# Optimization experiments

Hardware: AMD Instinct MI355X
Metric: run time of the kernel (lower is better)

Reference implementation:

```python
import jax, jax.numpy as jnp
import numpy as np

N_NODES = 100000
N_EDGES = 800000
DIMS = [(768, 64), (64, 32), (32, 16), (16, 5)]


def setup_inputs() -> dict:
    key = jax.random.key(0)
    ks = jax.random.split(key, 3 + 3 * len(DIMS))
    inp = {
        "x": jax.random.normal(ks[0], (N_NODES, DIMS[0][0]), jnp.float32),
        "edge_index": jax.random.randint(ks[1], (2, N_EDGES), 0, N_NODES),
        "edge_weight": jax.random.uniform(ks[2], (N_EDGES,), jnp.float32),
    }
    for i, (di, do) in enumerate(DIMS, start=1):
        s = 1.0 / np.sqrt(di)
        k0, k1, k2 = ks[3 * i], ks[3 * i + 1], ks[3 * i + 2]
        inp[f"W{i}l"] = jax.random.uniform(k0, (di, do), jnp.float32, -s, s)
        inp[f"W{i}r"] = jax.random.uniform(k1, (di, do), jnp.float32, -s, s)
        inp[f"b{i}"] = jax.random.uniform(k2, (do,), jnp.float32, -s, s)
    return inp


def _sage_conv(h, src, dst, inv_deg, Wl, Wr, b):
    # SAGEConv (mean aggregation): lin_l(mean_{j->i} h_j) + lin_r(h_i)
    agg = jax.ops.segment_sum(h[src], dst, num_segments=h.shape[0]) * inv_deg[:, None]
    return agg @ Wl + h @ Wr + b


def reference(x, edge_index, edge_weight,
              W1l, W1r, b1, W2l, W2r, b2, W3l, W3r, b3, W4l, W4r, b4):
    # edge_weight is accepted (matches original forward) but PyG SAGEConv mean
    # aggregation ignores it. Dropout is identity (deterministic eval reference).
    src, dst = edge_index[0], edge_index[1]
    deg = jax.ops.segment_sum(jnp.ones((src.shape[0],), x.dtype), dst,
                              num_segments=x.shape[0])
    inv_deg = jnp.where(deg > 0, 1.0 / deg, 0.0)
    h = jax.nn.relu(_sage_conv(x, src, dst, inv_deg, W1l, W1r, b1))
    h = jax.nn.relu(_sage_conv(h, src, dst, inv_deg, W2l, W2r, b2))
    h = jax.nn.relu(_sage_conv(h, src, dst, inv_deg, W3l, W3r, b3))
    return _sage_conv(h, src, dst, inv_deg, W4l, W4r, b4)
```

## Files before the change

kernel.cpp:

```cpp
#include <hip/hip_runtime.h>

using half8 = __attribute__((ext_vector_type(8))) _Float16;
using f32x4 = __attribute__((ext_vector_type(4))) float;

typedef __attribute__((address_space(3))) unsigned int lds_uint;
typedef __attribute__((address_space(1))) const unsigned int glb_uint;
__device__ __forceinline__ void async_copy16(const void* g, void* l) {
  __builtin_amdgcn_global_load_lds((glb_uint*)g, (lds_uint*)l, 16, 0, 0);
}

__device__ __forceinline__ void raw_barrier() {
  asm volatile("" ::: "memory");
  __builtin_amdgcn_s_barrier();
  asm volatile("" ::: "memory");
}

__global__ void zero_kernel(int4* __restrict__ p, int n4) {
  int i = blockIdx.x * 256 + threadIdx.x;
  if (i < n4) p[i] = make_int4(0, 0, 0, 0);
}

__global__ void prep_all_kernel(const float* __restrict__ W1l, const float* __restrict__ W1r,
                                const float* __restrict__ W2l, const float* __restrict__ W2r,
                                const float* __restrict__ W3l, const float* __restrict__ W3r,
                                const float* __restrict__ W4l, const float* __restrict__ W4r,
                                _Float16* __restrict__ w1, _Float16* __restrict__ w2,
                                _Float16* __restrict__ w3, _Float16* __restrict__ w4) {
  int i = blockIdx.x * 256 + threadIdx.x;
  if (i < 98304) {
    int c = i / 768, k = i - c * 768;
    float v = (c < 64) ? W1l[k * 64 + c] : W1r[k * 64 + (c - 64)];
    w1[i] = (_Float16)v;
  } else if (i < 98304 + 4096) {
    int j = i - 98304;
    int c = j >> 6, k = j & 63;
    float v = (c < 32) ? W2l[k * 32 + c] : W2r[k * 32 + (c - 32)];
    w2[j] = (_Float16)v;
  } else if (i < 98304 + 4096 + 1024) {
    int j = i - (98304 + 4096);
    int c = j >> 5, k = j & 31;
    float v = (c < 16) ? W3l[k * 16 + c] : W3r[k * 16 + (c - 16)];
    w3[j] = (_Float16)v;
  } else if (i < 98304 + 4096 + 1024 + 512) {
    int j = i - (98304 + 4096 + 1024);
    int c = j >> 5, k = j & 31;
    float v = 0.f;
    if (k < 16) {
      if (c < 5) v = W4l[k * 5 + c];
      else if (c < 10) v = W4r[k * 5 + (c - 5)];
    }
    w4[j] = (_Float16)v;
  }
}

__global__ void deg_kernel(const int* __restrict__ dst, int* __restrict__ cnt, int e) {
  int i = blockIdx.x * 256 + threadIdx.x;
  if (i < e) atomicAdd(&cnt[dst[i]], 1);
}

__global__ void scan1_kernel(const int* __restrict__ cnt, int* __restrict__ off,
                             int* __restrict__ bsum, float* __restrict__ invd, int nodes) {
  __shared__ int sh[256];
  int tid = threadIdx.x;
  int base = blockIdx.x * 1024 + tid * 4;
  int a0 = (base + 0 < nodes) ? cnt[base + 0] : 0;
  int a1 = (base + 1 < nodes) ? cnt[base + 1] : 0;
  int a2 = (base + 2 < nodes) ? cnt[base + 2] : 0;
  int a3 = (base + 3 < nodes) ? cnt[base + 3] : 0;
  if (base + 0 < nodes) invd[base + 0] = a0 > 0 ? 1.0f / (float)a0 : 0.f;
  if (base + 1 < nodes) invd[base + 1] = a1 > 0 ? 1.0f / (float)a1 : 0.f;
  if (base + 2 < nodes) invd[base + 2] = a2 > 0 ? 1.0f / (float)a2 : 0.f;
  if (base + 3 < nodes) invd[base + 3] = a3 > 0 ? 1.0f / (float)a3 : 0.f;
  int s3 = a0 + a1 + a2 + a3;
  sh[tid] = s3;
  __syncthreads();
  for (int d = 1; d < 256; d <<= 1) {
    int v = (tid >= d) ? sh[tid - d] : 0;
    __syncthreads();
    sh[tid] += v;
    __syncthreads();
  }
  int excl = sh[tid] - s3;
  if (base + 0 <= nodes) off[base + 0] = excl;
  if (base + 1 <= nodes) off[base + 1] = excl + a0;
  if (base + 2 <= nodes) off[base + 2] = excl + a0 + a1;
  if (base + 3 <= nodes) off[base + 3] = excl + a0 + a1 + a2;
  if (tid == 255) bsum[blockIdx.x] = sh[255];
}

__global__ void scan2_kernel(int* __restrict__ bsum, int nb) {
  __shared__ int sh[128];
  int tid = threadIdx.x;
  int v = (tid < nb) ? bsum[tid] : 0;
  sh[tid] = v;
  __syncthreads();
  for (int d = 1; d < 128; d <<= 1) {
    int u = (tid >= d) ? sh[tid - d] : 0;
    __syncthreads();
    sh[tid] += u;
    __syncthreads();
  }
  if (tid < nb) bsum[tid] = sh[tid] - v;
}

__global__ void scan3_kernel(int* __restrict__ off, const int* __restrict__ bsum, int ntot) {
  int i = blockIdx.x * 256 + threadIdx.x;
  if (i < ntot) off[i] += bsum[i >> 10];
}

__global__ void sortfill_kernel(const int* __restrict__ src, const int* __restrict__ dst,
                                const int* __restrict__ off, int* __restrict__ cur,
                                int* __restrict__ csr, int e) {
  int i = blockIdx.x * 256 + threadIdx.x;
  if (i < e) {
    int d = dst[i];
    int pos = atomicAdd(&cur[d], 1);
    csr[off[d] + pos] = src[i];
  }
}

__global__ __launch_bounds__(256, 3) void gemm1_kernel(
    const float* __restrict__ x,
    const _Float16* __restrict__ w16,
    const float* __restrict__ bias,
    _Float16* __restrict__ p, _Float16* __restrict__ q, int n) {
  constexpr int DI = 768, BK = 32, NT = DI / BK;
  __shared__ float aS[2][128 * BK];
  __shared__ _Float16 bS[2][128 * BK];
  int t = threadIdx.x;
  int lane = t & 63, w = t >> 6;
  int lm = lane & 15, lk = lane >> 4;
  int m0 = blockIdx.x * 128;

  const float* agp[4];
  int abase[4];
#pragma unroll
  for (int j = 0; j < 4; ++j) {
    int g = (j * 4 + w) * 64 + lane;
    int row = g >> 3, gi = g & 7;
    int gj = gi ^ (row & 7);
    int grow = m0 + row;
    if (grow >= n) grow = n - 1;
    agp[j] = x + (size_t)grow * DI + gj * 4;
    abase[j] = (j * 4 + w) * 256;
  }
  const _Float16* bgp[2];
  int bbase[2];
#pragma unroll
  for (int j = 0; j < 2; ++j) {
    int g = (j * 4 + w) * 64 + lane;
    int c = g >> 2, gi = g & 3;
    int gj = gi ^ ((c >> 1) & 3);
    bgp[j] = w16 + (size_t)c * DI + gj * 8;
    bbase[j] = (j * 4 + w) * 512;
  }

  f32x4 acc[2][8];
#pragma unroll
  for (int mi = 0; mi < 2; ++mi)
#pragma unroll
    for (int ni = 0; ni < 8; ++ni) acc[mi][ni] = (f32x4){0.f, 0.f, 0.f, 0.f};

  int r0l = w * 32 + lm, r1l = r0l + 16;
  int sw = lm & 7;
  int bsw = (lk ^ ((lm >> 1) & 3)) << 3;

  auto compute_tile = [&](const float* ab, const _Float16* bb) {
    f32x4 v0a = *(const f32x4*)(ab + r0l * 32 + (((lk * 2 + 0) ^ sw) << 2));
    f32x4 v0b = *(const f32x4*)(ab + r0l * 32 + (((lk * 2 + 1) ^ sw) << 2));
    f32x4 v1a = *(const f32x4*)(ab + r1l * 32 + (((lk * 2 + 0) ^ sw) << 2));
    f32x4 v1b = *(const f32x4*)(ab + r1l * 32 + (((lk * 2 + 1) ^ sw) << 2));
    half8 a0, a1;
#pragma unroll
    for (int j = 0; j < 4; ++j) {
      a0[j] = (_Float16)v0a[j]; a0[4 + j] = (_Float16)v0b[j];
      a1[j] = (_Float16)v1a[j]; a1[4 + j] = (_Float16)v1b[j];
    }
#pragma unroll
    for (int ni = 0; ni < 8; ++ni) {
      half8 b = *(const half8*)(bb + ni * 512 + lm * 32 + bsw);
      acc[0][ni] = __builtin_amdgcn_mfma_f32_16x16x32_f16(a0, b, acc[0][ni], 0, 0, 0);
      acc[1][ni] = __builtin_amdgcn_mfma_f32_16x16x32_f16(a1, b, acc[1][ni], 0, 0, 0);
    }
  };

#pragma unroll
  for (int j = 0; j < 4; ++j) async_copy16(agp[j], &aS[0][abase[j]]);
#pragma unroll
  for (int j = 0; j < 2; ++j) async_copy16(bgp[j], &bS[0][bbase[j]]);

  for (int ts = 0; ts < NT - 1; ++ts) {
    int cur = ts & 1;
    int kc = (ts + 1) * BK;
#pragma unroll
    for (int j = 0; j < 4; ++j) async_copy16(agp[j] + kc, &aS[cur ^ 1][abase[j]]);
#pragma unroll
    for (int j = 0; j < 2; ++j) async_copy16(bgp[j] + kc, &bS[cur ^ 1][bbase[j]]);
    asm volatile("s_waitcnt vmcnt(6)" ::: "memory");
    raw_barrier();
    compute_tile(aS[cur], bS[cur]);
    raw_barrier();
  }
  asm volatile("s_waitcnt vmcnt(0)" ::: "memory");
  raw_barrier();
  compute_tile(aS[(NT - 1) & 1], bS[(NT - 1) & 1]);

#pragma unroll
  for (int mi = 0; mi < 2; ++mi)
#pragma unroll
    for (int ni = 0; ni < 8; ++ni) {
      int col = ni * 16 + lm;
#pragma unroll
      for (int j = 0; j < 4; ++j) {
        int row = m0 + w * 32 + mi * 16 + lk * 4 + j;
        if (row < n) {
          float v = acc[mi][ni][j];
          if (col < 64) p[(size_t)row * 64 + col] = (_Float16)v;
          else q[(size_t)row * 64 + (col - 64)] = (_Float16)(v + bias[col - 64]);
        }
      }
    }
}

template <int DIR, int DIP, int PSI, int NC, int NCR, int DO, int PSO>
__global__ __launch_bounds__(256) void fused_agg_gemm_kernel(
    const _Float16* __restrict__ pin, const _Float16* __restrict__ qin,
    const int* __restrict__ off, const int* __restrict__ csr, const float* __restrict__ invd,
    const _Float16* __restrict__ w16, const float* __restrict__ bias,
    _Float16* __restrict__ pout, _Float16* __restrict__ qout, int n) {
  constexpr int SP = DIP + 8;
  constexpr int C8 = DIR / 8;
  constexpr int CT = C8 / 2;
  constexpr int NF = NC / 16;
  __shared__ _Float16 hs[128 * SP];
  int t = threadIdx.x;
  int node_l = t >> 1, half = t & 1;
  int node = blockIdx.x * 128 + node_l;

  if (node < n) {
    int e0 = off[node], e1 = off[node + 1];
    const half8* p8 = (const half8*)pin;
    float s[CT][8];
#pragma unroll
    for (int c = 0; c < CT; ++c)
#pragma unroll
      for (int j = 0; j < 8; ++j) s[c][j] = 0.f;
    for (int e = e0; e < e1; ++e) {
      int src = csr[e];
#pragma unroll
      for (int c = 0; c < CT; ++c) {
        half8 v = p8[(size_t)src * PSI + half * CT + c];
#pragma unroll
        for (int j = 0; j < 8; ++j) s[c][j] += (float)v[j];
      }
    }
    float id = invd[node];
#pragma unroll
    for (int c = 0; c < CT; ++c) {
      half8 qv = ((const half8*)qin)[(size_t)node * PSI + half * CT + c];
      half8 o;
#pragma unroll
      for (int j = 0; j < 8; ++j) o[j] = (_Float16)fmaxf(s[c][j] * id + (float)qv[j], 0.f);
      *(half8*)(hs + node_l * SP + (half * CT + c) * 8) = o;
    }
    if (DIP > DIR) {
      half8 z = {};
      *(half8*)(hs + node_l * SP + (C8 + half) * 8) = z;
    }
  }
  __syncthreads();

  int lane = t & 63, w = t >> 6;
  int lm = lane & 15, lk = lane >> 4;
  int r0l = w * 32 + lm, r1l = r0l + 16;
  const _Float16* wp = w16 + (size_t)lm * DIP + lk * 8;
  f32x4 acc[2][NF];
#pragma unroll
  for (int mi = 0; mi < 2; ++mi)
#pragma unroll
    for (int ni = 0; ni < NF; ++ni) acc[mi][ni] = (f32x4){0.f, 0.f, 0.f, 0.f};
#pragma unroll
  for (int kc = 0; kc < DIP; kc += 32) {
    half8 a0 = *(const half8*)(hs + r0l * SP + kc + lk * 8);
    half8 a1 = *(const half8*)(hs + r1l * SP + kc + lk * 8);
#pragma unroll
    for (int ni = 0; ni < NF; ++ni) {
      half8 b = *(const half8*)(wp + (size_t)ni * 16 * DIP + kc);
      acc[0][ni] = __builtin_amdgcn_mfma_f32_16x16x32_f16(a0, b, acc[0][ni], 0, 0, 0);
      acc[1][ni] = __builtin_amdgcn_mfma_f32_16x16x32_f16(a1, b, acc[1][ni], 0, 0, 0);
    }
  }
#pragma unroll
  for (int mi = 0; mi < 2; ++mi)
#pragma unroll
    for (int ni = 0; ni < NF; ++ni) {
      int col = ni * 16 + lm;
      if (col >= NCR) continue;
#pragma unroll
      for (int j = 0; j < 4; ++j) {
        int row = blockIdx.x * 128 + w * 32 + mi * 16 + lk * 4 + j;
        if (row < n) {
          float v = acc[mi][ni][j];
          if (col < DO) pout[(size_t)row * PSO + col] = (_Float16)v;
          else qout[(size_t)row * PSO + (col - DO)] = (_Float16)(v + bias[col - DO]);
        }
      }
    }
}

__global__ __launch_bounds__(256) void aggregate_last_kernel(
    const _Float16* __restrict__ p, const _Float16* __restrict__ q,
    const int* __restrict__ off, const int* __restrict__ csr,
    const float* __restrict__ invd, float* __restrict__ out, int n) {
  int t = blockIdx.x * 256 + threadIdx.x;
  int node = t >> 3;
  int c = t & 7;
  if (node >= n || c >= 5) return;
  int e0 = off[node], e1 = off[node + 1];
  float s = 0.f;
  for (int e = e0; e < e1; ++e) s += (float)p[(size_t)csr[e] * 8 + c];
  out[(size_t)node * 5 + c] = s * invd[node] + (float)q[(size_t)node * 8 + c];
}

extern "C" void kernel_launch(void* const* d_in, const int* in_sizes, int n_in,
                              void* d_out, int out_size, void* d_ws, size_t ws_size,
                              hipStream_t stream) {
  const float* x = (const float*)d_in[0];
  const int* ei = (const int*)d_in[1];
  const int E = in_sizes[1] / 2;
  const int* esrc = ei;
  const int* edst = ei + E;
  const float* W1l = (const float*)d_in[3];
  const float* W1r = (const float*)d_in[4];
  const float* b1 = (const float*)d_in[5];
  const float* W2l = (const float*)d_in[6];
  const float* W2r = (const float*)d_in[7];
  const float* b2 = (const float*)d_in[8];
  const float* W3l = (const float*)d_in[9];
  const float* W3r = (const float*)d_in[10];
  const float* b3 = (const float*)d_in[11];
  const float* W4l = (const float*)d_in[12];
  const float* W4r = (const float*)d_in[13];
  const float* b4 = (const float*)d_in[14];
  const int N = in_sizes[0] / 768;
  float* out = (float*)d_out;
  (void)n_in; (void)out_size; (void)ws_size;

  char* base = (char*)d_ws;
  size_t o = 0;
  auto alloc = [&](size_t bytes) -> void* {
    void* ptr = base + o;
    o = (o + bytes + 255) & ~(size_t)255;
    return ptr;
  };
  int* cnt = (int*)alloc((size_t)2 * N * 4);
  int* cur = cnt + N;
  int* off = (int*)alloc((size_t)(N + 1) * 4);
  int* bsum = (int*)alloc(1024);
  int* csr = (int*)alloc((size_t)E * 4);
  float* invd = (float*)alloc((size_t)N * 4);
  _Float16* w1 = (_Float16*)alloc((size_t)128 * 768 * 2);
  _Float16* w2 = (_Float16*)alloc((size_t)64 * 64 * 2);
  _Float16* w3 = (_Float16*)alloc((size_t)32 * 32 * 2);
  _Float16* w4 = (_Float16*)alloc((size_t)16 * 32 * 2);
  _Float16* P1 = (_Float16*)alloc((size_t)N * 64 * 2);
  _Float16* Q1 = (_Float16*)alloc((size_t)N * 64 * 2);
  _Float16* P2 = (_Float16*)alloc((size_t)N * 32 * 2);
  _Float16* Q2 = (_Float16*)alloc((size_t)N * 32 * 2);
  _Float16* P3 = (_Float16*)alloc((size_t)N * 16 * 2);
  _Float16* Q3 = (_Float16*)alloc((size_t)N * 16 * 2);
  _Float16* P4 = (_Float16*)alloc((size_t)N * 8 * 2);
  _Float16* Q4 = (_Float16*)alloc((size_t)N * 8 * 2);

  const int n4 = (2 * N + 3) / 4;
  zero_kernel<<<(n4 + 255) / 256, 256, 0, stream>>>((int4*)cnt, n4);
  prep_all_kernel<<<(98304 + 4096 + 1024 + 512 + 255) / 256, 256, 0, stream>>>(
      W1l, W1r, W2l, W2r, W3l, W3r, W4l, W4r, w1, w2, w3, w4);

  deg_kernel<<<(E + 255) / 256, 256, 0, stream>>>(edst, cnt, E);
  const int nb = (N + 1 + 1023) / 1024;
  scan1_kernel<<<nb, 256, 0, stream>>>(cnt, off, bsum, invd, N);
  scan2_kernel<<<1, 128, 0, stream>>>(bsum, nb);
  scan3_kernel<<<(N + 1 + 255) / 256, 256, 0, stream>>>(off, bsum, N + 1);
  sortfill_kernel<<<(E + 255) / 256, 256, 0, stream>>>(esrc, edst, off, cur, csr, E);

  const int gb = (N + 127) / 128;
  gemm1_kernel<<<gb, 256, 0, stream>>>(x, w1, b1, P1, Q1, N);
  fused_agg_gemm_kernel<64, 64, 8, 64, 64, 32, 32>
      <<<gb, 256, 0, stream>>>(P1, Q1, off, csr, invd, w2, b2, P2, Q2, N);
  fused_agg_gemm_kernel<32, 32, 4, 32, 32, 16, 16>
      <<<gb, 256, 0, stream>>>(P2, Q2, off, csr, invd, w3, b3, P3, Q3, N);
  fused_agg_gemm_kernel<16, 32, 2, 16, 10, 5, 8>
      <<<gb, 256, 0, stream>>>(P3, Q3, off, csr, invd, w4, b4, P4, Q4, N);
  aggregate_last_kernel<<<(N * 8 + 255) / 256, 256, 0, stream>>>(P4, Q4, off, csr, invd, out, N);
}
```

Baseline: 269.8 us.

## Triple-buffer gemm1 with 64-row tiles; unroll gather loops and vectorize last aggregation

```diff
diff --git a/kernel.cpp b/kernel.cpp
--- a/kernel.cpp
+++ b/kernel.cpp
@@ -125,101 +125,98 @@
     const float* __restrict__ bias,
     _Float16* __restrict__ p, _Float16* __restrict__ q, int n) {
   constexpr int DI = 768, BK = 32, NT = DI / BK;
-  __shared__ float aS[2][128 * BK];
-  __shared__ _Float16 bS[2][128 * BK];
+  __shared__ float aS[3][64 * BK];
+  __shared__ _Float16 bS[3][128 * BK];
   int t = threadIdx.x;
   int lane = t & 63, w = t >> 6;
   int lm = lane & 15, lk = lane >> 4;
-  int m0 = blockIdx.x * 128;
-
-  const float* agp[4];
-  int abase[4];
-#pragma unroll
-  for (int j = 0; j < 4; ++j) {
-    int g = (j * 4 + w) * 64 + lane;
+  int m0 = blockIdx.x * 64;
+
+  const float* agp[2];
+  int abase[2];
+#pragma unroll
+  for (int j = 0; j < 2; ++j) {
+    int g = j * 256 + w * 64 + lane;
     int row = g >> 3, gi = g & 7;
     int gj = gi ^ (row & 7);
     int grow = m0 + row;
     if (grow >= n) grow = n - 1;
     agp[j] = x + (size_t)grow * DI + gj * 4;
-    abase[j] = (j * 4 + w) * 256;
+    abase[j] = (j * 256 + w * 64) * 4;
   }
   const _Float16* bgp[2];
   int bbase[2];
 #pragma unroll
   for (int j = 0; j < 2; ++j) {
-    int g = (j * 4 + w) * 64 + lane;
+    int g = j * 256 + w * 64 + lane;
     int c = g >> 2, gi = g & 3;
     int gj = gi ^ ((c >> 1) & 3);
     bgp[j] = w16 + (size_t)c * DI + gj * 8;
-    bbase[j] = (j * 4 + w) * 512;
-  }
-
-  f32x4 acc[2][8];
-#pragma unroll
-  for (int mi = 0; mi < 2; ++mi)
-#pragma unroll
-    for (int ni = 0; ni < 8; ++ni) acc[mi][ni] = (f32x4){0.f, 0.f, 0.f, 0.f};
-
-  int r0l = w * 32 + lm, r1l = r0l + 16;
-  int sw = lm & 7;
+    bbase[j] = (j * 256 + w * 64) * 8;
+  }
+
+  f32x4 acc[8];
+#pragma unroll
+  for (int ni = 0; ni < 8; ++ni) acc[ni] = (f32x4){0.f, 0.f, 0.f, 0.f};
+
+  int r0l = w * 16 + lm;
+  int sw = r0l & 7;
   int bsw = (lk ^ ((lm >> 1) & 3)) << 3;
+
+  auto stage = [&](int buf, int kc) {
+#pragma unroll
+    for (int j = 0; j < 2; ++j) async_copy16(agp[j] + kc, &aS[buf][abase[j]]);
+#pragma unroll
+    for (int j = 0; j < 2; ++j) async_copy16(bgp[j] + kc, &bS[buf][bbase[j]]);
+  };
 
   auto compute_tile = [&](const float* ab, const _Float16* bb) {
     f32x4 v0a = *(const f32x4*)(ab + r0l * 32 + (((lk * 2 + 0) ^ sw) << 2));
     f32x4 v0b = *(const f32x4*)(ab + r0l * 32 + (((lk * 2 + 1) ^ sw) << 2));
-    f32x4 v1a = *(const f32x4*)(ab + r1l * 32 + (((lk * 2 + 0) ^ sw) << 2));
-    f32x4 v1b = *(const f32x4*)(ab + r1l * 32 + (((lk * 2 + 1) ^ sw) << 2));
-    half8 a0, a1;
+    half8 a0;
 #pragma unroll
     for (int j = 0; j < 4; ++j) {
-      a0[j] = (_Float16)v0a[j]; a0[4 + j] = (_Float16)v0b[j];
-      a1[j] = (_Float16)v1a[j]; a1[4 + j] = (_Float16)v1b[j];
+      a0[j] = (_Float16)v0a[j];
+      a0[4 + j] = (_Float16)v0b[j];
     }
 #pragma unroll
     for (int ni = 0; ni < 8; ++ni) {
-      half8 b = *(const half8*)(bb + ni * 512 + lm * 32 + bsw);
-      acc[0][ni] = __builtin_amdgcn_mfma_f32_16x16x32_f16(a0, b, acc[0][ni], 0, 0, 0);
-      acc[1][ni] = __builtin_amdgcn_mfma_f32_16x16x32_f16(a1, b, acc[1][ni], 0, 0, 0);
+      half8 b = *(const half8*)(bb + (ni * 16 + lm) * 32 + bsw);
+      acc[ni] = __builtin_amdgcn_mfma_f32_16x16x32_f16(a0, b, acc[ni], 0, 0, 0);
     }
   };
 
-#pragma unroll
-  for (int j = 0; j < 4; ++j) async_copy16(agp[j], &aS[0][abase[j]]);
-#pragma unroll
-  for (int j = 0; j < 2; ++j) async_copy16(bgp[j], &bS[0][bbase[j]]);
-
-  for (int ts = 0; ts < NT - 1; ++ts) {
-    int cur = ts & 1;
-    int kc = (ts + 1) * BK;
-#pragma unroll
-    for (int j = 0; j < 4; ++j) async_copy16(agp[j] + kc, &aS[cur ^ 1][abase[j]]);
-#pragma unroll
-    for (int j = 0; j < 2; ++j) async_copy16(bgp[j] + kc, &bS[cur ^ 1][bbase[j]]);
-    asm volatile("s_waitcnt vmcnt(6)" ::: "memory");
+  stage(0, 0);
+  stage(1, BK);
+
+  for (int ts = 0; ts < NT; ++ts) {
+    if (ts + 2 < NT) {
+      stage((ts + 2) % 3, (ts + 2) * BK);
+      asm volatile("s_waitcnt vmcnt(8)" ::: "memory");
+    } else if (ts + 1 < NT) {
+      asm volatile("s_waitcnt vmcnt(4)" ::: "memory");
+    } else {
+      asm volatile("s_waitcnt vmcnt(0)" ::: "memory");
+    }
     raw_barrier();
+    int cur = ts % 3;
     compute_tile(aS[cur], bS[cur]);
     raw_barrier();
   }
-  asm volatile("s_waitcnt vmcnt(0)" ::: "memory");
-  raw_barrier();
-  compute_tile(aS[(NT - 1) & 1], bS[(NT - 1) & 1]);
-
-#pragma unroll
-  for (int mi = 0; mi < 2; ++mi)
-#pragma unroll
-    for (int ni = 0; ni < 8; ++ni) {
-      int col = ni * 16 + lm;
-#pragma unroll
-      for (int j = 0; j < 4; ++j) {
-        int row = m0 + w * 32 + mi * 16 + lk * 4 + j;
-        if (row < n) {
-          float v = acc[mi][ni][j];
-          if (col < 64) p[(size_t)row * 64 + col] = (_Float16)v;
-          else q[(size_t)row * 64 + (col - 64)] = (_Float16)(v + bias[col - 64]);
-        }
+
+#pragma unroll
+  for (int ni = 0; ni < 8; ++ni) {
+    int col = ni * 16 + lm;
+#pragma unroll
+    for (int j = 0; j < 4; ++j) {
+      int row = m0 + w * 16 + lk * 4 + j;
+      if (row < n) {
+        float v = acc[ni][j];
+        if (col < 64) p[(size_t)row * 64 + col] = (_Float16)v;
+        else q[(size_t)row * 64 + (col - 64)] = (_Float16)(v + bias[col - 64]);
       }
     }
+  }
 }
 
 template <int DIR, int DIP, int PSI, int NC, int NCR, int DO, int PSO>
@@ -245,11 +242,27 @@
     for (int c = 0; c < CT; ++c)
 #pragma unroll
       for (int j = 0; j < 8; ++j) s[c][j] = 0.f;
-    for (int e = e0; e < e1; ++e) {
-      int src = csr[e];
+    int e = e0;
+    for (; e + 2 <= e1; e += 2) {
+      int i0 = csr[e], i1 = csr[e + 1];
+      half8 v0[CT], v1[CT];
+#pragma unroll
+      for (int c = 0; c < CT; ++c) v0[c] = p8[(size_t)i0 * PSI + half * CT + c];
+#pragma unroll
+      for (int c = 0; c < CT; ++c) v1[c] = p8[(size_t)i1 * PSI + half * CT + c];
+#pragma unroll
+      for (int c = 0; c < CT; ++c)
+#pragma unroll
+        for (int j = 0; j < 8; ++j) {
+          s[c][j] += (float)v0[c][j];
+          s[c][j] += (float)v1[c][j];
+        }
+    }
+    if (e < e1) {
+      int i0 = csr[e];
 #pragma unroll
       for (int c = 0; c < CT; ++c) {
-        half8 v = p8[(size_t)src * PSI + half * CT + c];
+        half8 v = p8[(size_t)i0 * PSI + half * CT + c];
 #pragma unroll
         for (int j = 0; j < 8; ++j) s[c][j] += (float)v[j];
       }
@@ -312,14 +325,32 @@
     const _Float16* __restrict__ p, const _Float16* __restrict__ q,
     const int* __restrict__ off, const int* __restrict__ csr,
     const float* __restrict__ invd, float* __restrict__ out, int n) {
-  int t = blockIdx.x * 256 + threadIdx.x;
-  int node = t >> 3;
-  int c = t & 7;
-  if (node >= n || c >= 5) return;
+  int node = blockIdx.x * 256 + threadIdx.x;
+  if (node >= n) return;
   int e0 = off[node], e1 = off[node + 1];
-  float s = 0.f;
-  for (int e = e0; e < e1; ++e) s += (float)p[(size_t)csr[e] * 8 + c];
-  out[(size_t)node * 5 + c] = s * invd[node] + (float)q[(size_t)node * 8 + c];
+  const half8* p8 = (const half8*)p;
+  float s[8];
+#pragma unroll
+  for (int j = 0; j < 8; ++j) s[j] = 0.f;
+  int e = e0;
+  for (; e + 2 <= e1; e += 2) {
+    half8 v0 = p8[csr[e]];
+    half8 v1 = p8[csr[e + 1]];
+#pragma unroll
+    for (int j = 0; j < 8; ++j) {
+      s[j] += (float)v0[j];
+      s[j] += (float)v1[j];
+    }
+  }
+  if (e < e1) {
+    half8 v = p8[csr[e]];
+#pragma unroll
+    for (int j = 0; j < 8; ++j) s[j] += (float)v[j];
+  }
+  float id = invd[node];
+  half8 qv = ((const half8*)q)[node];
+#pragma unroll
+  for (int j = 0; j < 5; ++j) out[(size_t)node * 5 + j] = s[j] * id + (float)qv[j];
 }
 
 extern "C" void kernel_launch(void* const* d_in, const int* in_sizes, int n_in,
@@ -384,13 +415,13 @@
   scan3_kernel<<<(N + 1 + 255) / 256, 256, 0, stream>>>(off, bsum, N + 1);
   sortfill_kernel<<<(E + 255) / 256, 256, 0, stream>>>(esrc, edst, off, cur, csr, E);
 
+  gemm1_kernel<<<(N + 63) / 64, 256, 0, stream>>>(x, w1, b1, P1, Q1, N);
   const int gb = (N + 127) / 128;
-  gemm1_kernel<<<gb, 256, 0, stream>>>(x, w1, b1, P1, Q1, N);
   fused_agg_gemm_kernel<64, 64, 8, 64, 64, 32, 32>
       <<<gb, 256, 0, stream>>>(P1, Q1, off, csr, invd, w2, b2, P2, Q2, N);
   fused_agg_gemm_kernel<32, 32, 4, 32, 32, 16, 16>
       <<<gb, 256, 0, stream>>>(P2, Q2, off, csr, invd, w3, b3, P3, Q3, N);
   fused_agg_gemm_kernel<16, 32, 2, 16, 10, 5, 8>
       <<<gb, 256, 0, stream>>>(P3, Q3, off, csr, invd, w4, b4, P4, Q4, N);
-  aggregate_last_kernel<<<(N * 8 + 255) / 256, 256, 0, stream>>>(P4, Q4, off, csr, invd, out, N);
-}
+  aggregate_last_kernel<<<(N + 255) / 256, 256, 0, stream>>>(P4, Q4, off, csr, invd, out, N);
+}
```

Result: no change. 273.5 us (+1.4%).
